# Kernel tuning notes

Measured on AMD Instinct MI355X. Metric: run time of the kernel, lower is better.

Reference implementation:

```python
import jax, jax.numpy as jnp
import numpy as np

N_RAYS = 65536
N_SAMPLES = 96


def setup_inputs() -> dict:
    key = jax.random.key(0)
    k1, k2, k3 = jax.random.split(key, 3)
    rgb = jax.random.uniform(k1, (N_RAYS, N_SAMPLES, 3), dtype=jnp.float32)
    # SDF values near the surface, small magnitude
    sdf = jax.random.normal(k2, (N_RAYS, N_SAMPLES), dtype=jnp.float32) * 0.1
    # monotonically increasing sample depths along each ray
    z_vals = jnp.sort(
        jax.random.uniform(k3, (N_RAYS, N_SAMPLES), dtype=jnp.float32,
                           minval=0.1, maxval=5.0), axis=-1)
    return {"rgb": rgb, "sdf": sdf, "z_vals": z_vals, "beta": 10}


def reference(rgb, sdf, z_vals, beta):
    # sdf2alpha: alpha = 1 - exp(-beta * sigmoid(-sdf * beta))
    alpha = 1.0 - jnp.exp(-beta * jax.nn.sigmoid(-sdf * beta))  # [N, S]
    # exclusive cumprod of (1 - alpha + 1e-10): transmittance
    trans = jnp.cumprod(
        jnp.concatenate([jnp.ones_like(alpha[:, :1]), 1.0 - alpha + 1e-10],
                        axis=-1), axis=-1)[:, :-1]  # [N, S]
    weights = alpha * trans  # [N, S]
    rendered_rgb = jnp.sum(weights[..., None] * rgb, axis=-2)  # [N, 3]
    rendered_depth = jnp.sum(weights * z_vals, axis=-1)  # [N]
    return (rendered_depth, rendered_rgb, sdf, z_vals)
```

## Files before the change

### kernel.cpp

```cpp
#include <hip/hip_runtime.h>
#include <hip/hip_bf16.h>


#define SDFR_NS 96
#define SDFR_RPB 8

__global__ __launch_bounds__(256, 8) void sdf_render_kernel(
    const float4* __restrict__ rgb4,
    const float4* __restrict__ sdf4,
    const float4* __restrict__ z4,
    const int*    __restrict__ beta_p,
    float*  __restrict__ out_depth,
    float*  __restrict__ out_rgb,
    float4* __restrict__ out_sdf4,
    float4* __restrict__ out_z4,
    int n_rays)
{
    __shared__ float4 sz_s[384];
    __shared__ float4 rgb_s[576];

    const int t  = threadIdx.x;
    const int r0 = blockIdx.x * SDFR_RPB;

    const long base4  = (long)r0 * (SDFR_NS / 4);
    const long rbase4 = (long)r0 * (SDFR_NS * 3 / 4);

    const int f1 = t;
    const int f2 = (256 + t > 383) ? 383 : 256 + t;
    const int g1 = t;
    const int g2 = 256 + t;
    const int g3 = (512 + t > 575) ? 575 : 512 + t;

    const float4* p1 = (f1 < 192) ? (sdf4 + base4 + f1)
                                  : (z4   + base4 + (f1 - 192));
    const float4* p2 = (f2 < 192) ? (sdf4 + base4 + f2)
                                  : (z4   + base4 + (f2 - 192));

    const float4 va  = *p1;
    const float4 vb  = *p2;
    const float4 vc1 = rgb4[rbase4 + g1];
    const float4 vc2 = rgb4[rbase4 + g2];
    const float4 vc3 = rgb4[rbase4 + g3];

    int bi = *beta_p;
    float beta;
    if (bi > 1000000 || bi < -1000000) {
        union { int i; float f; } u; u.i = bi; beta = u.f;
    } else {
        beta = (float)bi;
    }

    float4* q1 = (f1 < 192) ? (out_sdf4 + base4 + f1)
                            : (out_z4   + base4 + (f1 - 192));
    float4* q2 = (f2 < 192) ? (out_sdf4 + base4 + f2)
                            : (out_z4   + base4 + (f2 - 192));
    *q1 = va;
    *q2 = vb;

    sz_s[f1]  = va;
    sz_s[f2]  = vb;
    rgb_s[g1] = vc1;
    rgb_s[g2] = vc2;
    rgb_s[g3] = vc3;

    __syncthreads();

    const int g   = t >> 5;
    const int l   = t & 31;
    const int ray = r0 + g;

    const float* szf  = (const float*)sz_s;
    const float* rgbf = (const float*)rgb_s;

    const int sb = g * SDFR_NS + 3 * l;
    const float s0 = szf[sb], s1 = szf[sb + 1], s2 = szf[sb + 2];
    const float z0 = szf[768 + sb], z1 = szf[768 + sb + 1], z2 = szf[768 + sb + 2];

    const int rb = g * (SDFR_NS * 3) + 9 * l;
    const float c0 = rgbf[rb + 0], c1 = rgbf[rb + 1], c2 = rgbf[rb + 2];
    const float c3 = rgbf[rb + 3], c4 = rgbf[rb + 4], c5 = rgbf[rb + 5];
    const float c6 = rgbf[rb + 6], c7 = rgbf[rb + 7], c8 = rgbf[rb + 8];

    const float e0 = __expf(-beta * __builtin_amdgcn_rcpf(1.0f + __expf(s0 * beta)));
    const float e1 = __expf(-beta * __builtin_amdgcn_rcpf(1.0f + __expf(s1 * beta)));
    const float e2 = __expf(-beta * __builtin_amdgcn_rcpf(1.0f + __expf(s2 * beta)));
    const float a0 = 1.0f - e0, t0 = e0 + 1e-10f;
    const float a1 = 1.0f - e1, t1 = e1 + 1e-10f;
    const float a2 = 1.0f - e2, t2 = e2 + 1e-10f;

    const float m = t0 * t1 * t2;
    float scan = m;
    #pragma unroll
    for (int d = 1; d < 32; d <<= 1) {
        float v = __shfl_up(scan, d, 32);
        if (l >= d) scan *= v;
    }
    float E = __shfl_up(scan, 1, 32);
    if (l == 0) E = 1.0f;

    const float w0 = a0 * E;
    const float w1 = a1 * E * t0;
    const float w2 = a2 * E * t0 * t1;

    float depth = w0 * z0 + w1 * z1 + w2 * z2;
    float r0acc = w0 * c0 + w1 * c3 + w2 * c6;
    float r1acc = w0 * c1 + w1 * c4 + w2 * c7;
    float r2acc = w0 * c2 + w1 * c5 + w2 * c8;

    #pragma unroll
    for (int d = 16; d >= 1; d >>= 1) {
        depth += __shfl_xor(depth, d, 32);
        r0acc += __shfl_xor(r0acc, d, 32);
        r1acc += __shfl_xor(r1acc, d, 32);
        r2acc += __shfl_xor(r2acc, d, 32);
    }

    if (l == 0 && ray < n_rays) {
        out_depth[ray]       = depth;
        out_rgb[ray * 3 + 0] = r0acc;
        out_rgb[ray * 3 + 1] = r1acc;
        out_rgb[ray * 3 + 2] = r2acc;
    }
}

extern "C" void kernel_launch(void* const* d_in, const int* in_sizes, int n_in,
                              void* d_out, int out_size, void* d_ws, size_t ws_size,
                              hipStream_t stream) {
    (void)n_in; (void)d_ws; (void)ws_size; (void)out_size;

    const float4* rgb4   = (const float4*)d_in[0];
    const float4* sdf4   = (const float4*)d_in[1];
    const float4* z4     = (const float4*)d_in[2];
    const int*    beta_p = (const int*)d_in[3];

    const int n_rays = in_sizes[1] / SDFR_NS;

    float* out_depth = (float*)d_out;
    float* out_rgb   = out_depth + n_rays;
    float* out_sdf   = out_rgb   + (size_t)n_rays * 3;
    float* out_z     = out_sdf   + (size_t)n_rays * SDFR_NS;

    const int grid = (n_rays + SDFR_RPB - 1) / SDFR_RPB;
    sdf_render_kernel<<<grid, 256, 0, stream>>>(
        rgb4, sdf4, z4, beta_p, out_depth, out_rgb,
        (float4*)out_sdf, (float4*)out_z, n_rays);
}
```

Baseline: 169.2 us.

## Load ray samples directly from global memory, drop LDS staging and barrier

Replaces the cooperative float4 load into shared memory plus __syncthreads with per-lane direct loads of three sdf/z values and nine rgb values as 12-byte structs. The sdf/z copy-through now writes from each lane's registers. This removes LDS traffic and the block barrier. In exchange, the global loads become 12-byte strided accesses that may coalesce less efficiently than the float4 pattern.

```diff
diff --git a/kernel.cpp b/kernel.cpp
--- a/kernel.cpp
+++ b/kernel.cpp
@@ -1,46 +1,35 @@
 #include <hip/hip_runtime.h>
-#include <hip/hip_bf16.h>
 
 
 #define SDFR_NS 96
-#define SDFR_RPB 8
+
+struct f3 { float x, y, z; };
 
 __global__ __launch_bounds__(256, 8) void sdf_render_kernel(
-    const float4* __restrict__ rgb4,
-    const float4* __restrict__ sdf4,
-    const float4* __restrict__ z4,
-    const int*    __restrict__ beta_p,
-    float*  __restrict__ out_depth,
-    float*  __restrict__ out_rgb,
-    float4* __restrict__ out_sdf4,
-    float4* __restrict__ out_z4,
+    const float* __restrict__ rgb,
+    const float* __restrict__ sdf,
+    const float* __restrict__ z_vals,
+    const int*   __restrict__ beta_p,
+    float* __restrict__ out_depth,
+    float* __restrict__ out_rgb,
+    float* __restrict__ out_sdf,
+    float* __restrict__ out_z,
     int n_rays)
 {
-    __shared__ float4 sz_s[384];
-    __shared__ float4 rgb_s[576];
+    const int tid = blockIdx.x * 256 + threadIdx.x;
+    const int ray = tid >> 5;
+    const int l   = tid & 31;
+    if (ray >= n_rays) return;
 
-    const int t  = threadIdx.x;
-    const int r0 = blockIdx.x * SDFR_RPB;
+    const long sb = (long)ray * SDFR_NS + 3 * l;
+    const long rb = (long)ray * (SDFR_NS * 3) + 9 * l;
 
-    const long base4  = (long)r0 * (SDFR_NS / 4);
-    const long rbase4 = (long)r0 * (SDFR_NS * 3 / 4);
-
-    const int f1 = t;
-    const int f2 = (256 + t > 383) ? 383 : 256 + t;
-    const int g1 = t;
-    const int g2 = 256 + t;
-    const int g3 = (512 + t > 575) ? 575 : 512 + t;
-
-    const float4* p1 = (f1 < 192) ? (sdf4 + base4 + f1)
-                                  : (z4   + base4 + (f1 - 192));
-    const float4* p2 = (f2 < 192) ? (sdf4 + base4 + f2)
-                                  : (z4   + base4 + (f2 - 192));
-
-    const float4 va  = *p1;
-    const float4 vb  = *p2;
-    const float4 vc1 = rgb4[rbase4 + g1];
-    const float4 vc2 = rgb4[rbase4 + g2];
-    const float4 vc3 = rgb4[rbase4 + g3];
+    const f3 sv = *(const f3*)(sdf    + sb);
+    const f3 zv = *(const f3*)(z_vals + sb);
+    const f3 ca = *(const f3*)(rgb + rb + 0);
+    const f3 cb = *(const f3*)(rgb + rb + 3);
+    const f3 cc = *(const f3*)(rgb + rb + 6);
+    __builtin_amdgcn_sched_barrier(0);
 
     int bi = *beta_p;
     float beta;
@@ -50,43 +39,15 @@
         beta = (float)bi;
     }
 
-    float4* q1 = (f1 < 192) ? (out_sdf4 + base4 + f1)
-                            : (out_z4   + base4 + (f1 - 192));
-    float4* q2 = (f2 < 192) ? (out_sdf4 + base4 + f2)
-                            : (out_z4   + base4 + (f2 - 192));
-    *q1 = va;
-    *q2 = vb;
-
-    sz_s[f1]  = va;
-    sz_s[f2]  = vb;
-    rgb_s[g1] = vc1;
-    rgb_s[g2] = vc2;
-    rgb_s[g3] = vc3;
-
-    __syncthreads();
-
-    const int g   = t >> 5;
-    const int l   = t & 31;
-    const int ray = r0 + g;
-
-    const float* szf  = (const float*)sz_s;
-    const float* rgbf = (const float*)rgb_s;
-
-    const int sb = g * SDFR_NS + 3 * l;
-    const float s0 = szf[sb], s1 = szf[sb + 1], s2 = szf[sb + 2];
-    const float z0 = szf[768 + sb], z1 = szf[768 + sb + 1], z2 = szf[768 + sb + 2];
-
-    const int rb = g * (SDFR_NS * 3) + 9 * l;
-    const float c0 = rgbf[rb + 0], c1 = rgbf[rb + 1], c2 = rgbf[rb + 2];
-    const float c3 = rgbf[rb + 3], c4 = rgbf[rb + 4], c5 = rgbf[rb + 5];
-    const float c6 = rgbf[rb + 6], c7 = rgbf[rb + 7], c8 = rgbf[rb + 8];
-
-    const float e0 = __expf(-beta * __builtin_amdgcn_rcpf(1.0f + __expf(s0 * beta)));
-    const float e1 = __expf(-beta * __builtin_amdgcn_rcpf(1.0f + __expf(s1 * beta)));
-    const float e2 = __expf(-beta * __builtin_amdgcn_rcpf(1.0f + __expf(s2 * beta)));
+    const float e0 = __expf(-beta * __builtin_amdgcn_rcpf(1.0f + __expf(sv.x * beta)));
+    const float e1 = __expf(-beta * __builtin_amdgcn_rcpf(1.0f + __expf(sv.y * beta)));
+    const float e2 = __expf(-beta * __builtin_amdgcn_rcpf(1.0f + __expf(sv.z * beta)));
     const float a0 = 1.0f - e0, t0 = e0 + 1e-10f;
     const float a1 = 1.0f - e1, t1 = e1 + 1e-10f;
     const float a2 = 1.0f - e2, t2 = e2 + 1e-10f;
+
+    *(f3*)(out_sdf + sb) = sv;
+    *(f3*)(out_z   + sb) = zv;
 
     const float m = t0 * t1 * t2;
     float scan = m;
@@ -102,24 +63,23 @@
     const float w1 = a1 * E * t0;
     const float w2 = a2 * E * t0 * t1;
 
-    float depth = w0 * z0 + w1 * z1 + w2 * z2;
-    float r0acc = w0 * c0 + w1 * c3 + w2 * c6;
-    float r1acc = w0 * c1 + w1 * c4 + w2 * c7;
-    float r2acc = w0 * c2 + w1 * c5 + w2 * c8;
+    float depth = w0 * zv.x + w1 * zv.y + w2 * zv.z;
+    float r0    = w0 * ca.x + w1 * cb.x + w2 * cc.x;
+    float r1    = w0 * ca.y + w1 * cb.y + w2 * cc.y;
+    float r2    = w0 * ca.z + w1 * cb.z + w2 * cc.z;
 
     #pragma unroll
     for (int d = 16; d >= 1; d >>= 1) {
         depth += __shfl_xor(depth, d, 32);
-        r0acc += __shfl_xor(r0acc, d, 32);
-        r1acc += __shfl_xor(r1acc, d, 32);
-        r2acc += __shfl_xor(r2acc, d, 32);
+        r0    += __shfl_xor(r0, d, 32);
+        r1    += __shfl_xor(r1, d, 32);
+        r2    += __shfl_xor(r2, d, 32);
     }
 
-    if (l == 0 && ray < n_rays) {
-        out_depth[ray]       = depth;
-        out_rgb[ray * 3 + 0] = r0acc;
-        out_rgb[ray * 3 + 1] = r1acc;
-        out_rgb[ray * 3 + 2] = r2acc;
+    if (l == 0) {
+        out_depth[ray] = depth;
+        f3 o; o.x = r0; o.y = r1; o.z = r2;
+        *(f3*)(out_rgb + (long)ray * 3) = o;
     }
 }
 
@@ -128,10 +88,10 @@
                               hipStream_t stream) {
     (void)n_in; (void)d_ws; (void)ws_size; (void)out_size;
 
-    const float4* rgb4   = (const float4*)d_in[0];
-    const float4* sdf4   = (const float4*)d_in[1];
-    const float4* z4     = (const float4*)d_in[2];
-    const int*    beta_p = (const int*)d_in[3];
+    const float* rgb    = (const float*)d_in[0];
+    const float* sdf    = (const float*)d_in[1];
+    const float* z      = (const float*)d_in[2];
+    const int*   beta_p = (const int*)d_in[3];
 
     const int n_rays = in_sizes[1] / SDFR_NS;
 
@@ -140,8 +100,8 @@
     float* out_sdf   = out_rgb   + (size_t)n_rays * 3;
     float* out_z     = out_sdf   + (size_t)n_rays * SDFR_NS;
 
-    const int grid = (n_rays + SDFR_RPB - 1) / SDFR_RPB;
+    const long total_threads = (long)n_rays * 32;
+    const int  grid = (int)((total_threads + 255) / 256);
     sdf_render_kernel<<<grid, 256, 0, stream>>>(
-        rgb4, sdf4, z4, beta_p, out_depth, out_rgb,
-        (float4*)out_sdf, (float4*)out_z, n_rays);
+        rgb, sdf, z, beta_p, out_depth, out_rgb, out_sdf, out_z, n_rays);
 }
```

New measurement: 170.8 us. About the same (+1.0%).
